# Kernel optimization log

Measured on AMD Instinct MI355X. Metric: run time of the kernel, lower is better.

## Reference

```python
import jax, jax.numpy as jnp
import numpy as np

BLOCK_SIZE = 128  # config.block_size; first query block skips intra-block causal mask (faithful to source)
NEG = -1e9       # the module uses -1e9, not -inf, for masking and m_i init


def setup_inputs() -> dict:
    key = jax.random.key(0)
    kq, kk, kv, km = jax.random.split(key, 4)
    B, S, H, D = 2, 2048, 16, 64
    q = jax.random.normal(kq, (B, S, H, D), dtype=jnp.float32)
    k = jax.random.normal(kk, (B, S, H, D), dtype=jnp.float32)
    v = jax.random.normal(kv, (B, S, H, D), dtype=jnp.float32)
    mask = jax.random.randint(km, (B, S), 0, 2).astype(bool)
    mask = mask.at[:, 0].set(True)  # keep first key attendable
    return {"q": q, "k": k, "v": v, "mask": mask}


def reference(q, k, v, mask):
    # q,k,v: [B,S,H,D]; mask: [B,S] bool (True = attend)
    B, S, H, D = q.shape
    scale = 1.0 / np.sqrt(D)
    # config.normalize_query=True -> F.normalize(q, dim=-1) (eps=1e-12)
    qn = q / jnp.maximum(jnp.linalg.norm(q, axis=-1, keepdims=True), 1e-12)
    # scores: [B,S(query),H,S(key)]
    scores = jnp.einsum('bshd,bkhd->bshk', qn, k) * scale
    qi = jnp.arange(S)[:, None]
    ki = jnp.arange(S)[None, :]
    # Faithful causal structure of the blocked PyTorch fallback:
    #  - keys limited to k <= q (triu(diagonal=block_start+1) masking)
    #  - EXCEPT the first query block (block_start==0), where the intra-block
    #    causal mask is skipped (keys still limited to the first block).
    allowed = (ki <= qi) | ((qi < BLOCK_SIZE) & (ki < BLOCK_SIZE))  # [S,S]
    scores = jnp.where(allowed[None, :, None, :], scores, NEG)
    scores = jnp.where(mask[:, None, None, :], scores, NEG)
    p = jax.nn.softmax(scores, axis=-1)
    out = jnp.einsum('bshk,bkhd->bshd', p, v)
    return out
```

## Files before the change

kernel.cpp:

```cpp
#include <hip/hip_runtime.h>
#include <stdint.h>

typedef __attribute__((ext_vector_type(8))) short short8;
typedef __attribute__((ext_vector_type(4))) float floatx4;
typedef __attribute__((ext_vector_type(4))) unsigned int uintx4;
typedef __attribute__((ext_vector_type(2))) unsigned int uintx2;

#define S_LEN 2048
#define NHEAD 16
#define DHEAD 64
#define KB    64
#define NTILE 32
#define PL_BYTES (S_LEN * DHEAD * 2)
#define VOFF  (2 * NHEAD * PL_BYTES)
#define MOFF  (2 * VOFF)
#define POFF  (MOFF + 8192)
#define DOFF  (POFF + 1024 * 16384)
#define WS_NEEDED ((size_t)DOFF + 1024 * 256)
#define NEGINF (-__builtin_inff())
#define LOG2E 1.4426950408889634f

#define GLOAD_LDS16(gp, lp) \
    __builtin_amdgcn_global_load_lds((const __attribute__((address_space(1))) unsigned int*)(gp), \
                                     (__attribute__((address_space(3))) unsigned int*)(lp), 16, 0, 0)

static __device__ __forceinline__ unsigned f2bf(float f) {
    union { float f; unsigned u; } w; w.f = f;
    return (w.u + 0x7FFFu + ((w.u >> 16) & 1u)) >> 16;
}

static __device__ __forceinline__ unsigned cvtpk(float lo, float hi) {
    unsigned r;
    asm("v_cvt_pk_bf16_f32 %0, %1, %2" : "=v"(r) : "v"(lo), "v"(hi));
    return r;
}

static __device__ __forceinline__ floatx4 mfma16(short8 a, short8 b, floatx4 c) {
    return __builtin_amdgcn_mfma_f32_16x16x32_bf16(a, b, c, 0, 0, 0);
}

__global__ __launch_bounds__(256) void prep_kernel(
    const float* __restrict__ kg, const float* __restrict__ vg,
    const int* __restrict__ mg, char* __restrict__ ws)
{
    __shared__ unsigned short Tl[64 * 72];
    const int bid = blockIdx.x;
    const int t   = bid & 31;
    const int bh  = bid >> 5;
    const int b   = bh >> 4, h = bh & 15;
    const int tid = threadIdx.x;
    char* kpre = ws + (size_t)bh * PL_BYTES;
    char* vpre = ws + VOFF + (size_t)bh * PL_BYTES;

    {
        const int r  = tid >> 2;
        const int c0 = (tid & 3) * 32;
        const int X  = (r & 7) << 4;
        const size_t grow = (((size_t)b * S_LEN + t * 64 + r) * NHEAD + h) * DHEAD;
        #pragma unroll
        for (int cc = 0; cc < 2; ++cc) {
            const int c  = c0 + 16 * cc;
            const int d0 = (c ^ X) >> 1;
            floatx4 f0 = *(const floatx4*)(kg + grow + d0);
            floatx4 f1 = *(const floatx4*)(kg + grow + d0 + 4);
            uintx4 pk = (uintx4){ f2bf(f0[0]) | (f2bf(f0[1]) << 16),
                                  f2bf(f0[2]) | (f2bf(f0[3]) << 16),
                                  f2bf(f1[0]) | (f2bf(f1[1]) << 16),
                                  f2bf(f1[2]) | (f2bf(f1[3]) << 16) };
            *(uintx4*)(kpre + t * 8192 + r * 128 + c) = pk;
        }
    }
    {
        const int key = tid >> 2;
        const int d0  = (tid & 3) * 16;
        const float vz = mg[(size_t)b * S_LEN + t * 64 + key] ? 1.f : 0.f;
        const size_t grow = (((size_t)b * S_LEN + t * 64 + key) * NHEAD + h) * DHEAD;
        #pragma unroll
        for (int q = 0; q < 4; ++q) {
            floatx4 f = *(const floatx4*)(vg + grow + d0 + 4 * q);
            #pragma unroll
            for (int ii = 0; ii < 4; ++ii)
                Tl[(d0 + 4 * q + ii) * 72 + key] = (unsigned short)f2bf(f[ii] * vz);
        }
    }
    __syncthreads();
    {
        const int d  = tid >> 2;
        const int c0 = (tid & 3) * 32;
        const int Xv = (d & 7) << 4;
        #pragma unroll
        for (int cc = 0; cc < 2; ++cc) {
            const int c   = c0 + 16 * cc;
            const int pp0 = (c ^ Xv) >> 1;
            const int blk = pp0 >> 5;
            const int a   = (pp0 & 31) >> 3;
            unsigned short vals[8];
            #pragma unroll
            for (int i = 0; i < 8; ++i) {
                const int key = 32 * blk + ((i < 4) ? (4 * a + i) : (16 + 4 * a + i - 4));
                vals[i] = Tl[d * 72 + key];
            }
            *(uintx4*)(vpre + t * 8192 + d * 128 + c) = *(const uintx4*)vals;
        }
    }
    if (h == 0 && tid < 64) {
        const int key = tid;
        const int gg = (key >> 2) & 3, lo = key & 3;
        const int ks = key >> 5,      hi = (key >> 4) & 1;
        const unsigned short mv = mg[(size_t)b * S_LEN + t * 64 + key] ? 0x3F80 : 0;
        *(unsigned short*)(ws + MOFF + (size_t)b * 4096 + t * 128
                           + gg * 32 + ks * 16 + (4 * hi + lo) * 2) = mv;
    }
}

__global__ __launch_bounds__(256, 4) void fa3_main(
    const float* __restrict__ qg, char* __restrict__ ws,
    float* __restrict__ og)
{
    __shared__ char smem[40960];
    unsigned short* Qs = (unsigned short*)smem;
    char* KsB = smem + 8192;
    char* VsB = smem + 24576;

    const int tid  = threadIdx.x;
    const int bid  = blockIdx.x;
    int a, bh, chunk;
    if (bid < 1024) { a = 31 - (bid >> 6); chunk = (bid >> 5) & 1; bh = bid & 31; }
    else            { int r = bid - 1024; a = 15 - (r >> 5); chunk = 0; bh = r & 31; }
    const int b    = bh >> 4;
    const int h    = bh & 15;
    const int w    = tid >> 6;
    const int lane = tid & 63;
    const int g    = lane >> 4;
    const int lm   = lane & 15;
    const int kh   = w >> 1;
    const int wq   = w & 1;
    const char* kpre = ws + (size_t)bh * PL_BYTES;
    const char* vpre = ws + VOFF + (size_t)bh * PL_BYTES;
    const char* mgf  = ws + MOFF + (size_t)b * 4096;

    const int nktTot = (a < 2) ? 2 : (a + 1);
    const bool split = (a >= 16);
    int kt0, kt1;
    if (split) {
        const int h1 = nktTot >> 1, h0 = nktTot - h1;
        kt0 = chunk ? h0 : 0;  kt1 = chunk ? nktTot : h0;
    } else { kt0 = 0; kt1 = nktTot; }

    {
        const size_t tb = (size_t)kt0 * 8192;
        GLOAD_LDS16(kpre + tb + tid * 16,        KsB + tid * 16);
        GLOAD_LDS16(kpre + tb + 4096 + tid * 16, KsB + 4096 + tid * 16);
        GLOAD_LDS16(vpre + tb + tid * 16,        VsB + tid * 16);
        GLOAD_LDS16(vpre + tb + 4096 + tid * 16, VsB + 4096 + tid * 16);
    }

    {
        const int r  = tid >> 2;
        const int q0 = tid & 3;
        const float* src = qg + (((size_t)b * S_LEN + (size_t)a * 64 + r) * NHEAD + h) * DHEAD + q0 * 16;
        floatx4 f0 = *(const floatx4*)(src + 0);
        floatx4 f1 = *(const floatx4*)(src + 4);
        floatx4 f2 = *(const floatx4*)(src + 8);
        floatx4 f3 = *(const floatx4*)(src + 12);
        float ssq = 0.f;
        #pragma unroll
        for (int i = 0; i < 4; ++i)
            ssq += f0[i]*f0[i] + f1[i]*f1[i] + f2[i]*f2[i] + f3[i]*f3[i];
        ssq += __shfl_xor(ssq, 1);
        ssq += __shfl_xor(ssq, 2);
        const float sc = (0.125f * LOG2E) / fmaxf(sqrtf(ssq), 1e-12f);
        float fv[16];
        #pragma unroll
        for (int i = 0; i < 4; ++i) { fv[i]=f0[i]; fv[4+i]=f1[i]; fv[8+i]=f2[i]; fv[12+i]=f3[i]; }
        unsigned pk[8];
        #pragma unroll
        for (int i = 0; i < 8; ++i)
            pk[i] = cvtpk(fv[2*i]*sc, fv[2*i+1]*sc);
        const int X = (r & 7) << 4;
        char* qp = (char*)Qs + r * 128;
        *(uintx4*)(qp + ((32*q0)      ^ X)) = (uintx4){pk[0],pk[1],pk[2],pk[3]};
        *(uintx4*)(qp + ((32*q0 + 16) ^ X)) = (uintx4){pk[4],pk[5],pk[6],pk[7]};
    }
    asm volatile("s_waitcnt vmcnt(0)" ::: "memory");
    __syncthreads();

    const int Xl = (lm & 7) << 4;
    short8 qf[2][2];
    #pragma unroll
    for (int grp = 0; grp < 2; ++grp) {
        const int row = wq * 32 + grp * 16 + lm;
        const char* base = (const char*)Qs + row * 128;
        #pragma unroll
        for (int ksd = 0; ksd < 2; ++ksd)
            qf[grp][ksd] = *(const short8*)(base + ((64*ksd + 16*g) ^ Xl));
    }

    floatx4 oacc[2][4];
    floatx4 dacc[2];
    #pragma unroll
    for (int grp = 0; grp < 2; ++grp) {
        dacc[grp] = (floatx4){0.f,0.f,0.f,0.f};
        #pragma unroll
        for (int nt = 0; nt < 4; ++nt) oacc[grp][nt] = (floatx4){0.f,0.f,0.f,0.f};
    }
    floatx4 NEG8 = (floatx4){-8.f,-8.f,-8.f,-8.f};
    asm volatile("" : "+v"(NEG8));
    const int qgl0 = a * 64 + wq * 32 + lm;

    int cur = 0;
    for (int kt = kt0; kt < kt1; ++kt) {
        if (kt + 1 < kt1) {
            const size_t tb = (size_t)(kt + 1) * 8192;
            char* kb = KsB + (cur ^ 1) * 8192;
            char* vb = VsB + (cur ^ 1) * 8192;
            GLOAD_LDS16(kpre + tb + tid * 16,        kb + tid * 16);
            GLOAD_LDS16(kpre + tb + 4096 + tid * 16, kb + 4096 + tid * 16);
            GLOAD_LDS16(vpre + tb + tid * 16,        vb + tid * 16);
            GLOAD_LDS16(vpre + tb + 4096 + tid * 16, vb + 4096 + tid * 16);
        }
        const short8 mf = *(const short8*)(mgf + kt * 128 + g * 32 + kh * 16);

        floatx4 st[2][2];
        const char* kbase = KsB + cur * 8192 + kh * 4096 + lm * 128;
        __builtin_amdgcn_s_setprio(1);
        #pragma unroll
        for (int mt = 0; mt < 2; ++mt) {
            short8 kf = *(const short8*)(kbase + mt * 2048 + ((16*g) ^ Xl));
            st[0][mt] = mfma16(kf, qf[0][0], NEG8);
            st[1][mt] = mfma16(kf, qf[1][0], NEG8);
        }
        #pragma unroll
        for (int mt = 0; mt < 2; ++mt) {
            short8 kf = *(const short8*)(kbase + mt * 2048 + ((64 + 16*g) ^ Xl));
            st[0][mt] = mfma16(kf, qf[0][1], st[0][mt]);
            st[1][mt] = mfma16(kf, qf[1][1], st[1][mt]);
        }
        __builtin_amdgcn_s_setprio(0);

        if ((a >= 2) && (kt == a)) {
            #pragma unroll
            for (int mt = 0; mt < 2; ++mt)
                #pragma unroll
                for (int j = 0; j < 4; ++j) {
                    const int kgl = kt * KB + kh * 32 + mt * 16 + 4 * g + j;
                    if (kgl > qgl0)      st[0][mt][j] = -10000.f;
                    if (kgl > qgl0 + 16) st[1][mt][j] = -10000.f;
                }
        }

        short8 pa[2];
        #pragma unroll
        for (int grp = 0; grp < 2; ++grp) {
            float p[8];
            #pragma unroll
            for (int mt = 0; mt < 2; ++mt)
                #pragma unroll
                for (int j = 0; j < 4; ++j)
                    p[mt * 4 + j] = exp2f(st[grp][mt][j]);
            union { short8 s; uintx4 u; } pu;
            pu.u = (uintx4){ cvtpk(p[0], p[1]), cvtpk(p[2], p[3]),
                             cvtpk(p[4], p[5]), cvtpk(p[6], p[7]) };
            pa[grp] = pu.s;
        }
        __builtin_amdgcn_s_setprio(1);
        dacc[0] = mfma16(pa[0], mf, dacc[0]);
        dacc[1] = mfma16(pa[1], mf, dacc[1]);
        {
            const char* vbase = VsB + cur * 8192 + lm * 128;
            #pragma unroll
            for (int nt = 0; nt < 4; ++nt) {
                short8 vf = *(const short8*)(vbase + nt * 2048 + ((64*kh + 16*g) ^ Xl));
                oacc[0][nt] = mfma16(pa[0], vf, oacc[0][nt]);
                oacc[1][nt] = mfma16(pa[1], vf, oacc[1][nt]);
            }
        }
        __builtin_amdgcn_s_setprio(0);

        asm volatile("s_waitcnt vmcnt(0)" ::: "memory");
        __syncthreads();
        cur ^= 1;
    }

    floatx4* rbuf = (floatx4*)(smem + 8192);
    float*   dbuf = (float*)smem;
    if (kh == 1) {
        #pragma unroll
        for (int grp = 0; grp < 2; ++grp)
            #pragma unroll
            for (int nt = 0; nt < 4; ++nt)
                rbuf[((grp * 4 + nt) * 2 + wq) * 64 + lane] = oacc[grp][nt];
    }
    __syncthreads();
    if (kh == 0) {
        #pragma unroll
        for (int grp = 0; grp < 2; ++grp)
            #pragma unroll
            for (int nt = 0; nt < 4; ++nt)
                oacc[grp][nt] += rbuf[((grp * 4 + nt) * 2 + wq) * 64 + lane];
    }
    __syncthreads();
    if (kh == 1 && lm == 0) {
        #pragma unroll
        for (int grp = 0; grp < 2; ++grp)
            #pragma unroll
            for (int j = 0; j < 4; ++j)
                dbuf[wq * 32 + grp * 16 + 4 * g + j] = dacc[grp][j];
    }
    __syncthreads();
    if (kh == 0) {
        if (!split) {
            #pragma unroll
            for (int grp = 0; grp < 2; ++grp)
                #pragma unroll
                for (int j = 0; j < 4; ++j) {
                    const int rl = wq * 32 + grp * 16 + 4 * g + j;
                    const float invj = 1.0f / (dacc[grp][j] + dbuf[rl]);
                    float* dst = og + (((size_t)b * S_LEN + a * 64 + rl) * NHEAD + h) * DHEAD + lm;
                    #pragma unroll
                    for (int nt = 0; nt < 4; ++nt) dst[nt * 16] = oacc[grp][nt][j] * invj;
                }
        } else {
            const int s = (((a & 15) * 32 + bh) << 1) | chunk;
            float* po = (float*)(ws + POFF + (size_t)s * 16384);
            float* pd = (float*)(ws + DOFF + (size_t)s * 256);
            #pragma unroll
            for (int grp = 0; grp < 2; ++grp)
                #pragma unroll
                for (int j = 0; j < 4; ++j) {
                    const int rl = wq * 32 + grp * 16 + 4 * g + j;
                    #pragma unroll
                    for (int nt = 0; nt < 4; ++nt)
                        po[rl * 64 + nt * 16 + lm] = oacc[grp][nt][j];
                    if (lm == 0) pd[rl] = dacc[grp][j] + dbuf[rl];
                }
        }
    }
}

__global__ __launch_bounds__(256) void fa3_combine(
    const char* __restrict__ ws, float* __restrict__ og)
{
    const int i0  = (blockIdx.x * 256 + threadIdx.x) * 8;
    const int d   = i0 & 63;
    const int row = (i0 >> 6) & 63;
    const int bh  = (i0 >> 12) & 31;
    const int ai  = i0 >> 17;
    const int b   = bh >> 4, h = bh & 15;
    const int s0  = ((ai * 32 + bh) << 1);
    const float* p0 = (const float*)(ws + POFF + (size_t)s0 * 16384) + row * 64 + d;
    const float* p1 = (const float*)(ws + POFF + (size_t)(s0 + 1) * 16384) + row * 64 + d;
    const float den = ((const float*)(ws + DOFF + (size_t)s0 * 256))[row]
                    + ((const float*)(ws + DOFF + (size_t)(s0 + 1) * 256))[row];
    const float inv = 1.0f / den;
    floatx4 a0 = *(const floatx4*)p0, a1 = *(const floatx4*)(p0 + 4);
    floatx4 b0 = *(const floatx4*)p1, b1 = *(const floatx4*)(p1 + 4);
    floatx4 o0, o1;
    #pragma unroll
    for (int i = 0; i < 4; ++i) { o0[i] = (a0[i] + b0[i]) * inv; o1[i] = (a1[i] + b1[i]) * inv; }
    float* dst = og + (((size_t)b * S_LEN + (16 + ai) * 64 + row) * NHEAD + h) * DHEAD + d;
    *(floatx4*)dst       = o0;
    *(floatx4*)(dst + 4) = o1;
}

__global__ __launch_bounds__(512) void fa3_fallback(
    const float* __restrict__ qg, const float* __restrict__ kg,
    const float* __restrict__ vg, const int* __restrict__ mg,
    float* __restrict__ og)
{
    __shared__ unsigned short Qs[128 * DHEAD];
    __shared__ unsigned short Ks2[KB * DHEAD];
    __shared__ unsigned short Vt[DHEAD * KB];
    __shared__ float Ms[KB];

    const int tid  = threadIdx.x;
    const int bid  = blockIdx.x;
    const int qb   = 15 - (bid >> 5);
    const int bh   = bid & 31;
    const int b    = bh >> 4;
    const int h    = bh & 15;
    const int w    = tid >> 6;
    const int lane = tid & 63;
    const int g    = lane >> 4;
    const int lm   = lane & 15;

    {
        const int r  = tid >> 2;
        const int q0 = tid & 3;
        const float* src = qg + (((size_t)b * S_LEN + (size_t)qb * 128 + r) * NHEAD + h) * DHEAD + q0 * 16;
        floatx4 f0 = *(const floatx4*)(src + 0);
        floatx4 f1 = *(const floatx4*)(src + 4);
        floatx4 f2 = *(const floatx4*)(src + 8);
        floatx4 f3 = *(const floatx4*)(src + 12);
        float ssq = 0.f;
        #pragma unroll
        for (int i = 0; i < 4; ++i)
            ssq += f0[i]*f0[i] + f1[i]*f1[i] + f2[i]*f2[i] + f3[i]*f3[i];
        ssq += __shfl_xor(ssq, 1);
        ssq += __shfl_xor(ssq, 2);
        const float sc = 0.125f / fmaxf(sqrtf(ssq), 1e-12f);
        float fv[16];
        #pragma unroll
        for (int i = 0; i < 4; ++i) { fv[i]=f0[i]; fv[4+i]=f1[i]; fv[8+i]=f2[i]; fv[12+i]=f3[i]; }
        unsigned pk[8];
        #pragma unroll
        for (int i = 0; i < 8; ++i)
            pk[i] = f2bf(fv[2*i]*sc) | (f2bf(fv[2*i+1]*sc) << 16);
        const int X = (r & 7) << 4;
        char* qp = (char*)Qs + r * 128;
        *(uintx4*)(qp + ((32*q0)      ^ X)) = (uintx4){pk[0],pk[1],pk[2],pk[3]};
        *(uintx4*)(qp + ((32*q0 + 16) ^ X)) = (uintx4){pk[4],pk[5],pk[6],pk[7]};
    }
    __syncthreads();

    short8 qf[2];
    {
        const int row = w * 16 + lm;
        const int X = (row & 7) << 4;
        const char* base = (const char*)Qs + row * 128;
        #pragma unroll
        for (int ks = 0; ks < 2; ++ks) {
            union { short8 s; uintx2 u[2]; } u;
            u.u[0] = *(const uintx2*)(base + ((64*ks + 8*g)      ^ X));
            u.u[1] = *(const uintx2*)(base + ((64*ks + 8*g + 32) ^ X));
            qf[ks] = u.s;
        }
    }

    floatx4 oacc[4];
    #pragma unroll
    for (int nt = 0; nt < 4; ++nt) oacc[nt] = (floatx4){0.f,0.f,0.f,0.f};
    float mrun = NEGINF, lrun = 0.f;
    const int q_glob = qb * 128 + w * 16 + lm;
    const int nkt = (qb == 0) ? 2 : (2 * qb + 2);

    for (int kt = 0; kt < nkt; ++kt) {
        const int kb0 = kt * KB;
        {
            const int r = tid >> 3;
            const int o = tid & 7;
            const size_t goff = (((size_t)b * S_LEN + kb0 + r) * NHEAD + h) * DHEAD + o * 8;
            floatx4 a0 = *(const floatx4*)(kg + goff);
            floatx4 a1 = *(const floatx4*)(kg + goff + 4);
            floatx4 c0 = *(const floatx4*)(vg + goff);
            floatx4 c1 = *(const floatx4*)(vg + goff + 4);
            uintx4 kw = (uintx4){ f2bf(a0[0]) | (f2bf(a0[1])<<16),
                                  f2bf(a0[2]) | (f2bf(a0[3])<<16),
                                  f2bf(a1[0]) | (f2bf(a1[1])<<16),
                                  f2bf(a1[2]) | (f2bf(a1[3])<<16) };
            *(uintx4*)((char*)Ks2 + r*128 + ((16*o) ^ ((r & 7) << 4))) = kw;
            float cv[8];
            #pragma unroll
            for (int i = 0; i < 4; ++i) { cv[i] = c0[i]; cv[4+i] = c1[i]; }
            #pragma unroll
            for (int i = 0; i < 8; ++i) {
                const int d = 8*o + i;
                Vt[d*64 + (r ^ (((i ^ o) & 7) << 3))] = (unsigned short)f2bf(cv[i]);
            }
            if (tid < KB) Ms[tid] = mg[(size_t)b * S_LEN + kb0 + tid] ? 0.f : NEGINF;
        }
        __syncthreads();

        floatx4 st[4];
        #pragma unroll
        for (int mt = 0; mt < 4; ++mt) st[mt] = (floatx4){0.f,0.f,0.f,0.f};
        #pragma unroll
        for (int ks = 0; ks < 2; ++ks) {
            #pragma unroll
            for (int mt = 0; mt < 4; ++mt) {
                const int row = mt * 16 + lm;
                const int X = (row & 7) << 4;
                const char* base = (const char*)Ks2 + row * 128;
                union { short8 s; uintx2 u[2]; } u;
                u.u[0] = *(const uintx2*)(base + ((64*ks + 8*g)      ^ X));
                u.u[1] = *(const uintx2*)(base + ((64*ks + 8*g + 32) ^ X));
                st[mt] = mfma16(u.s, qf[ks], st[mt]);
            }
        }

        const bool diag = (qb > 0) && (kt >= 2 * qb);
        float sv[16];
        #pragma unroll
        for (int mt = 0; mt < 4; ++mt) {
            #pragma unroll
            for (int j = 0; j < 4; ++j) {
                const int kl = mt * 16 + 4 * g + j;
                float s = st[mt][j] + Ms[kl];
                if (diag && (kb0 + kl > q_glob)) s = NEGINF;
                sv[mt * 4 + j] = s;
            }
        }

        float rmax = sv[0];
        #pragma unroll
        for (int i = 1; i < 16; ++i) rmax = fmaxf(rmax, sv[i]);
        rmax = fmaxf(rmax, __shfl_xor(rmax, 16));
        rmax = fmaxf(rmax, __shfl_xor(rmax, 32));
        const float mnew = fmaxf(mrun, rmax);
        const float cf = __expf(mrun - mnew);
        float p[16], psum = 0.f;
        #pragma unroll
        for (int i = 0; i < 16; ++i) { p[i] = __expf(sv[i] - mnew); psum += p[i]; }
        psum += __shfl_xor(psum, 16);
        psum += __shfl_xor(psum, 32);
        lrun = lrun * cf + psum;
        mrun = mnew;

        float cj[4];
        #pragma unroll
        for (int j = 0; j < 4; ++j) cj[j] = __shfl(cf, 20 * g + j);
        #pragma unroll
        for (int nt = 0; nt < 4; ++nt)
            #pragma unroll
            for (int j = 0; j < 4; ++j) oacc[nt][j] *= cj[j];

        short8 pa[2];
        #pragma unroll
        for (int ks = 0; ks < 2; ++ks)
            #pragma unroll
            for (int i = 0; i < 8; ++i)
                pa[ks][i] = (short)f2bf(p[(2*ks + (i>>2))*4 + (i&3)]);

        #pragma unroll
        for (int nt = 0; nt < 4; ++nt) {
            const int d = 16 * nt + lm;
            const int xz = (((d & 7) ^ ((d >> 3) & 7)) & 7) << 4;
            const char* vb = (const char*)Vt + d * 128;
            #pragma unroll
            for (int ks = 0; ks < 2; ++ks) {
                union { short8 s; uintx2 u[2]; } vu;
                vu.u[0] = *(const uintx2*)(vb + ((64*ks + 8*g)      ^ xz));
                vu.u[1] = *(const uintx2*)(vb + ((64*ks + 8*g + 32) ^ xz));
                oacc[nt] = mfma16(pa[ks], vu.s, oacc[nt]);
            }
        }
        __syncthreads();
    }

    const float inv = 1.0f / lrun;
    #pragma unroll
    for (int j = 0; j < 4; ++j) {
        const float invj = __shfl(inv, 20 * g + j);
        const int row = qb * 128 + w * 16 + 4 * g + j;
        float* dst = og + (((size_t)b * S_LEN + row) * NHEAD + h) * DHEAD + lm;
        #pragma unroll
        for (int nt = 0; nt < 4; ++nt) dst[nt * 16] = oacc[nt][j] * invj;
    }
}

extern "C" void kernel_launch(void* const* d_in, const int* in_sizes, int n_in,
                              void* d_out, int out_size, void* d_ws, size_t ws_size,
                              hipStream_t stream)
{
    const float* q = (const float*)d_in[0];
    const float* k = (const float*)d_in[1];
    const float* v = (const float*)d_in[2];
    const int*   m = (const int*)d_in[3];
    float* out = (float*)d_out;
    (void)in_sizes; (void)n_in; (void)out_size;
    if (ws_size >= WS_NEEDED) {
        prep_kernel<<<dim3(1024), dim3(256), 0, stream>>>(k, v, m, (char*)d_ws);
        fa3_main<<<dim3(1536), dim3(256), 0, stream>>>(q, (char*)d_ws, out);
        fa3_combine<<<dim3(1024), dim3(256), 0, stream>>>((const char*)d_ws, out);
    } else {
        fa3_fallback<<<dim3(512), dim3(512), 0, stream>>>(q, k, v, m, out);
    }
}
```

Measured before the change: 52.66 us.

## Use FP8 QK^T MFMA with 128-row query blocks and 512-thread workgroups

```diff
diff --git a/kernel.cpp b/kernel.cpp
--- a/kernel.cpp
+++ b/kernel.cpp
@@ -10,15 +10,16 @@
 #define NHEAD 16
 #define DHEAD 64
 #define KB    64
-#define NTILE 32
-#define PL_BYTES (S_LEN * DHEAD * 2)
-#define VOFF  (2 * NHEAD * PL_BYTES)
-#define MOFF  (2 * VOFF)
+#define KPL   131072
+#define VPL   262144
+#define VOFF  (32 * KPL)
+#define MOFF  (VOFF + 32 * VPL)
 #define POFF  (MOFF + 8192)
-#define DOFF  (POFF + 1024 * 16384)
-#define WS_NEEDED ((size_t)DOFF + 1024 * 256)
+#define DOFF  (POFF + 512 * 32768)
+#define WS_NEEDED ((size_t)DOFF + 512 * 512)
 #define NEGINF (-__builtin_inff())
 #define LOG2E 1.4426950408889634f
+#define CSC   0.011271055f
 
 #define GLOAD_LDS16(gp, lp) \
     __builtin_amdgcn_global_load_lds((const __attribute__((address_space(1))) unsigned int*)(gp), \
@@ -28,15 +29,20 @@
     union { float f; unsigned u; } w; w.f = f;
     return (w.u + 0x7FFFu + ((w.u >> 16) & 1u)) >> 16;
 }
-
 static __device__ __forceinline__ unsigned cvtpk(float lo, float hi) {
     unsigned r;
     asm("v_cvt_pk_bf16_f32 %0, %1, %2" : "=v"(r) : "v"(lo), "v"(hi));
     return r;
 }
-
+template <int HI>
+static __device__ __forceinline__ int cvtfp8(float a, float b, int old) {
+    return __builtin_amdgcn_cvt_pk_fp8_f32(a, b, old, HI);
+}
 static __device__ __forceinline__ floatx4 mfma16(short8 a, short8 b, floatx4 c) {
     return __builtin_amdgcn_mfma_f32_16x16x32_bf16(a, b, c, 0, 0, 0);
+}
+static __device__ __forceinline__ floatx4 mfma8(long a, long b, floatx4 c) {
+    return __builtin_amdgcn_mfma_f32_16x16x32_fp8_fp8(a, b, c, 0, 0, 0);
 }
 
 __global__ __launch_bounds__(256) void prep_kernel(
@@ -49,26 +55,27 @@
     const int bh  = bid >> 5;
     const int b   = bh >> 4, h = bh & 15;
     const int tid = threadIdx.x;
-    char* kpre = ws + (size_t)bh * PL_BYTES;
-    char* vpre = ws + VOFF + (size_t)bh * PL_BYTES;
+    char* kpre = ws + (size_t)bh * KPL;
+    char* vpre = ws + VOFF + (size_t)bh * VPL;
 
     {
         const int r  = tid >> 2;
-        const int c0 = (tid & 3) * 32;
-        const int X  = (r & 7) << 4;
-        const size_t grow = (((size_t)b * S_LEN + t * 64 + r) * NHEAD + h) * DHEAD;
-        #pragma unroll
-        for (int cc = 0; cc < 2; ++cc) {
-            const int c  = c0 + 16 * cc;
-            const int d0 = (c ^ X) >> 1;
-            floatx4 f0 = *(const floatx4*)(kg + grow + d0);
-            floatx4 f1 = *(const floatx4*)(kg + grow + d0 + 4);
-            uintx4 pk = (uintx4){ f2bf(f0[0]) | (f2bf(f0[1]) << 16),
-                                  f2bf(f0[2]) | (f2bf(f0[3]) << 16),
-                                  f2bf(f1[0]) | (f2bf(f1[1]) << 16),
-                                  f2bf(f1[2]) | (f2bf(f1[3]) << 16) };
-            *(uintx4*)(kpre + t * 8192 + r * 128 + c) = pk;
-        }
+        const int c4 = tid & 3;
+        const size_t grow = (((size_t)b * S_LEN + t * 64 + r) * NHEAD + h) * DHEAD + 16 * c4;
+        floatx4 f0 = *(const floatx4*)(kg + grow);
+        floatx4 f1 = *(const floatx4*)(kg + grow + 4);
+        floatx4 f2 = *(const floatx4*)(kg + grow + 8);
+        floatx4 f3 = *(const floatx4*)(kg + grow + 12);
+        int w0 = 0, w1 = 0, w2 = 0, w3 = 0;
+        w0 = cvtfp8<0>(f0[0], f0[1], w0); w0 = cvtfp8<1>(f0[2], f0[3], w0);
+        w1 = cvtfp8<0>(f1[0], f1[1], w1); w1 = cvtfp8<1>(f1[2], f1[3], w1);
+        w2 = cvtfp8<0>(f2[0], f2[1], w2); w2 = cvtfp8<1>(f2[2], f2[3], w2);
+        w3 = cvtfp8<0>(f3[0], f3[1], w3); w3 = cvtfp8<1>(f3[2], f3[3], w3);
+        const int Xr = r & 7;
+        char* dst = kpre + t * 4096 + r * 64 + 8 * (((2 * c4) ^ Xr) & ~1);
+        *(uintx4*)dst = (Xr & 1)
+            ? (uintx4){(unsigned)w2, (unsigned)w3, (unsigned)w0, (unsigned)w1}
+            : (uintx4){(unsigned)w0, (unsigned)w1, (unsigned)w2, (unsigned)w3};
     }
     {
         const int key = tid >> 2;
@@ -113,52 +120,44 @@
     }
 }
 
-__global__ __launch_bounds__(256, 4) void fa3_main(
+__global__ __launch_bounds__(512, 4) void fa3_main(
     const float* __restrict__ qg, char* __restrict__ ws,
     float* __restrict__ og)
 {
-    __shared__ char smem[40960];
-    unsigned short* Qs = (unsigned short*)smem;
+    __shared__ char smem[32768];
+    char* Qs  = smem;
     char* KsB = smem + 8192;
-    char* VsB = smem + 24576;
+    char* VsB = smem + 16384;
 
     const int tid  = threadIdx.x;
     const int bid  = blockIdx.x;
-    int a, bh, chunk;
-    if (bid < 1024) { a = 31 - (bid >> 6); chunk = (bid >> 5) & 1; bh = bid & 31; }
-    else            { int r = bid - 1024; a = 15 - (r >> 5); chunk = 0; bh = r & 31; }
+    const int gidx = bid >> 5;
+    const int bh   = bid & 31;
+    int qb, chunk; bool split;
+    if (gidx < 16) { qb = 15 - (gidx >> 1); chunk = gidx & 1; split = true; }
+    else           { qb = 7 - (gidx - 16);  chunk = 0;        split = false; }
     const int b    = bh >> 4;
     const int h    = bh & 15;
     const int w    = tid >> 6;
     const int lane = tid & 63;
     const int g    = lane >> 4;
     const int lm   = lane & 15;
-    const int kh   = w >> 1;
-    const int wq   = w & 1;
-    const char* kpre = ws + (size_t)bh * PL_BYTES;
-    const char* vpre = ws + VOFF + (size_t)bh * PL_BYTES;
+    const int kh   = w >> 2;
+    const int wq   = w & 3;
+    const char* kpre = ws + (size_t)bh * KPL;
+    const char* vpre = ws + VOFF + (size_t)bh * VPL;
     const char* mgf  = ws + MOFF + (size_t)b * 4096;
-
-    const int nktTot = (a < 2) ? 2 : (a + 1);
-    const bool split = (a >= 16);
-    int kt0, kt1;
-    if (split) {
-        const int h1 = nktTot >> 1, h0 = nktTot - h1;
-        kt0 = chunk ? h0 : 0;  kt1 = chunk ? nktTot : h0;
-    } else { kt0 = 0; kt1 = nktTot; }
-
-    {
-        const size_t tb = (size_t)kt0 * 8192;
-        GLOAD_LDS16(kpre + tb + tid * 16,        KsB + tid * 16);
-        GLOAD_LDS16(kpre + tb + 4096 + tid * 16, KsB + 4096 + tid * 16);
-        GLOAD_LDS16(vpre + tb + tid * 16,        VsB + tid * 16);
-        GLOAD_LDS16(vpre + tb + 4096 + tid * 16, VsB + 4096 + tid * 16);
-    }
+    const int nkt = (qb == 0) ? 2 : (2 * qb + 2);
+    int kt0 = 0, kt1 = nkt;
+    if (split) { const int hh = nkt >> 1; kt0 = chunk ? hh : 0; kt1 = chunk ? nkt : hh; }
+
+    if (tid < 256) GLOAD_LDS16(kpre + (size_t)kt0 * 4096 + tid * 16, KsB + tid * 16);
+    GLOAD_LDS16(vpre + (size_t)kt0 * 8192 + tid * 16, VsB + tid * 16);
 
     {
         const int r  = tid >> 2;
         const int q0 = tid & 3;
-        const float* src = qg + (((size_t)b * S_LEN + (size_t)a * 64 + r) * NHEAD + h) * DHEAD + q0 * 16;
+        const float* src = qg + (((size_t)b * S_LEN + (size_t)qb * 128 + r) * NHEAD + h) * DHEAD + q0 * 16;
         floatx4 f0 = *(const floatx4*)(src + 0);
         floatx4 f1 = *(const floatx4*)(src + 4);
         floatx4 f2 = *(const floatx4*)(src + 8);
@@ -169,31 +168,30 @@
             ssq += f0[i]*f0[i] + f1[i]*f1[i] + f2[i]*f2[i] + f3[i]*f3[i];
         ssq += __shfl_xor(ssq, 1);
         ssq += __shfl_xor(ssq, 2);
-        const float sc = (0.125f * LOG2E) / fmaxf(sqrtf(ssq), 1e-12f);
-        float fv[16];
-        #pragma unroll
-        for (int i = 0; i < 4; ++i) { fv[i]=f0[i]; fv[4+i]=f1[i]; fv[8+i]=f2[i]; fv[12+i]=f3[i]; }
-        unsigned pk[8];
-        #pragma unroll
-        for (int i = 0; i < 8; ++i)
-            pk[i] = cvtpk(fv[2*i]*sc, fv[2*i+1]*sc);
-        const int X = (r & 7) << 4;
-        char* qp = (char*)Qs + r * 128;
-        *(uintx4*)(qp + ((32*q0)      ^ X)) = (uintx4){pk[0],pk[1],pk[2],pk[3]};
-        *(uintx4*)(qp + ((32*q0 + 16) ^ X)) = (uintx4){pk[4],pk[5],pk[6],pk[7]};
+        const float sc = 16.0f / fmaxf(sqrtf(ssq), 1e-12f);
+        int w0 = 0, w1 = 0, w2 = 0, w3 = 0;
+        w0 = cvtfp8<0>(f0[0]*sc, f0[1]*sc, w0); w0 = cvtfp8<1>(f0[2]*sc, f0[3]*sc, w0);
+        w1 = cvtfp8<0>(f1[0]*sc, f1[1]*sc, w1); w1 = cvtfp8<1>(f1[2]*sc, f1[3]*sc, w1);
+        w2 = cvtfp8<0>(f2[0]*sc, f2[1]*sc, w2); w2 = cvtfp8<1>(f2[2]*sc, f2[3]*sc, w2);
+        w3 = cvtfp8<0>(f3[0]*sc, f3[1]*sc, w3); w3 = cvtfp8<1>(f3[2]*sc, f3[3]*sc, w3);
+        const int Xr = r & 7;
+        char* qp = Qs + r * 64 + 8 * (((2 * q0) ^ Xr) & ~1);
+        *(uintx4*)qp = (Xr & 1)
+            ? (uintx4){(unsigned)w2, (unsigned)w3, (unsigned)w0, (unsigned)w1}
+            : (uintx4){(unsigned)w0, (unsigned)w1, (unsigned)w2, (unsigned)w3};
     }
     asm volatile("s_waitcnt vmcnt(0)" ::: "memory");
     __syncthreads();
 
-    const int Xl = (lm & 7) << 4;
-    short8 qf[2][2];
+    const int Xl8  = (lm & 7) << 3;
+    const int Xl16 = (lm & 7) << 4;
+    long qf8[2][2];
     #pragma unroll
     for (int grp = 0; grp < 2; ++grp) {
-        const int row = wq * 32 + grp * 16 + lm;
-        const char* base = (const char*)Qs + row * 128;
+        const char* base = Qs + (wq * 32 + grp * 16 + lm) * 64;
         #pragma unroll
         for (int ksd = 0; ksd < 2; ++ksd)
-            qf[grp][ksd] = *(const short8*)(base + ((64*ksd + 16*g) ^ Xl));
+            qf8[grp][ksd] = *(const long*)(base + ((32 * ksd + 8 * g) ^ Xl8));
     }
 
     floatx4 oacc[2][4];
@@ -204,48 +202,46 @@
         #pragma unroll
         for (int nt = 0; nt < 4; ++nt) oacc[grp][nt] = (floatx4){0.f,0.f,0.f,0.f};
     }
-    floatx4 NEG8 = (floatx4){-8.f,-8.f,-8.f,-8.f};
-    asm volatile("" : "+v"(NEG8));
-    const int qgl0 = a * 64 + wq * 32 + lm;
+    floatx4 ZERO4 = (floatx4){0.f,0.f,0.f,0.f};
+    asm volatile("" : "+v"(ZERO4));
+    const int qgl0 = qb * 128 + wq * 32 + lm;
 
     int cur = 0;
     for (int kt = kt0; kt < kt1; ++kt) {
         if (kt + 1 < kt1) {
-            const size_t tb = (size_t)(kt + 1) * 8192;
-            char* kb = KsB + (cur ^ 1) * 8192;
-            char* vb = VsB + (cur ^ 1) * 8192;
-            GLOAD_LDS16(kpre + tb + tid * 16,        kb + tid * 16);
-            GLOAD_LDS16(kpre + tb + 4096 + tid * 16, kb + 4096 + tid * 16);
-            GLOAD_LDS16(vpre + tb + tid * 16,        vb + tid * 16);
-            GLOAD_LDS16(vpre + tb + 4096 + tid * 16, vb + 4096 + tid * 16);
+            if (tid < 256)
+                GLOAD_LDS16(kpre + (size_t)(kt + 1) * 4096 + tid * 16,
+                            KsB + (cur ^ 1) * 4096 + tid * 16);
+            GLOAD_LDS16(vpre + (size_t)(kt + 1) * 8192 + tid * 16,
+                        VsB + (cur ^ 1) * 8192 + tid * 16);
         }
         const short8 mf = *(const short8*)(mgf + kt * 128 + g * 32 + kh * 16);
 
         floatx4 st[2][2];
-        const char* kbase = KsB + cur * 8192 + kh * 4096 + lm * 128;
+        const char* kbase = KsB + cur * 4096 + kh * 2048 + lm * 64;
         __builtin_amdgcn_s_setprio(1);
         #pragma unroll
         for (int mt = 0; mt < 2; ++mt) {
-            short8 kf = *(const short8*)(kbase + mt * 2048 + ((16*g) ^ Xl));
-            st[0][mt] = mfma16(kf, qf[0][0], NEG8);
-            st[1][mt] = mfma16(kf, qf[1][0], NEG8);
+            long kf = *(const long*)(kbase + mt * 1024 + ((8 * g) ^ Xl8));
+            st[0][mt] = mfma8(kf, qf8[0][0], ZERO4);
+            st[1][mt] = mfma8(kf, qf8[1][0], ZERO4);
         }
         #pragma unroll
         for (int mt = 0; mt < 2; ++mt) {
-            short8 kf = *(const short8*)(kbase + mt * 2048 + ((64 + 16*g) ^ Xl));
-            st[0][mt] = mfma16(kf, qf[0][1], st[0][mt]);
-            st[1][mt] = mfma16(kf, qf[1][1], st[1][mt]);
+            long kf = *(const long*)(kbase + mt * 1024 + ((32 + 8 * g) ^ Xl8));
+            st[0][mt] = mfma8(kf, qf8[0][1], st[0][mt]);
+            st[1][mt] = mfma8(kf, qf8[1][1], st[1][mt]);
         }
         __builtin_amdgcn_s_setprio(0);
 
-        if ((a >= 2) && (kt == a)) {
+        if ((qb >= 1) && (kt >= 2 * qb)) {
             #pragma unroll
             for (int mt = 0; mt < 2; ++mt)
                 #pragma unroll
                 for (int j = 0; j < 4; ++j) {
                     const int kgl = kt * KB + kh * 32 + mt * 16 + 4 * g + j;
-                    if (kgl > qgl0)      st[0][mt][j] = -10000.f;
-                    if (kgl > qgl0 + 16) st[1][mt][j] = -10000.f;
+                    if (kgl > qgl0)      st[0][mt][j] = -1e6f;
+                    if (kgl > qgl0 + 16) st[1][mt][j] = -1e6f;
                 }
         }
 
@@ -257,7 +253,7 @@
             for (int mt = 0; mt < 2; ++mt)
                 #pragma unroll
                 for (int j = 0; j < 4; ++j)
-                    p[mt * 4 + j] = exp2f(st[grp][mt][j]);
+                    p[mt * 4 + j] = exp2f(fmaf(st[grp][mt][j], CSC, -8.0f));
             union { short8 s; uintx4 u; } pu;
             pu.u = (uintx4){ cvtpk(p[0], p[1]), cvtpk(p[2], p[3]),
                              cvtpk(p[4], p[5]), cvtpk(p[6], p[7]) };
@@ -270,7 +266,7 @@
             const char* vbase = VsB + cur * 8192 + lm * 128;
             #pragma unroll
             for (int nt = 0; nt < 4; ++nt) {
-                short8 vf = *(const short8*)(vbase + nt * 2048 + ((64*kh + 16*g) ^ Xl));
+                short8 vf = *(const short8*)(vbase + nt * 2048 + ((64 * kh + 16 * g) ^ Xl16));
                 oacc[0][nt] = mfma16(pa[0], vf, oacc[0][nt]);
                 oacc[1][nt] = mfma16(pa[1], vf, oacc[1][nt]);
             }
@@ -282,14 +278,14 @@
         cur ^= 1;
     }
 
-    floatx4* rbuf = (floatx4*)(smem + 8192);
+    floatx4* rbuf = (floatx4*)smem;
     float*   dbuf = (float*)smem;
     if (kh == 1) {
         #pragma unroll
         for (int grp = 0; grp < 2; ++grp)
             #pragma unroll
             for (int nt = 0; nt < 4; ++nt)
-                rbuf[((grp * 4 + nt) * 2 + wq) * 64 + lane] = oacc[grp][nt];
+                rbuf[((grp * 4 + nt) * 4 + wq) * 64 + lane] = oacc[grp][nt];
     }
     __syncthreads();
     if (kh == 0) {
@@ -297,7 +293,7 @@
         for (int grp = 0; grp < 2; ++grp)
             #pragma unroll
             for (int nt = 0; nt < 4; ++nt)
-                oacc[grp][nt] += rbuf[((grp * 4 + nt) * 2 + wq) * 64 + lane];
+                oacc[grp][nt] += rbuf[((grp * 4 + nt) * 4 + wq) * 64 + lane];
     }
     __syncthreads();
     if (kh == 1 && lm == 0) {
@@ -316,14 +312,14 @@
                 for (int j = 0; j < 4; ++j) {
                     const int rl = wq * 32 + grp * 16 + 4 * g + j;
                     const float invj = 1.0f / (dacc[grp][j] + dbuf[rl]);
-                    float* dst = og + (((size_t)b * S_LEN + a * 64 + rl) * NHEAD + h) * DHEAD + lm;
+                    float* dst = og + (((size_t)b * S_LEN + qb * 128 + rl) * NHEAD + h) * DHEAD + lm;
                     #pragma unroll
                     for (int nt = 0; nt < 4; ++nt) dst[nt * 16] = oacc[grp][nt][j] * invj;
                 }
         } else {
-            const int s = (((a & 15) * 32 + bh) << 1) | chunk;
-            float* po = (float*)(ws + POFF + (size_t)s * 16384);
-            float* pd = (float*)(ws + DOFF + (size_t)s * 256);
+            const int s = ((qb - 8) * 32 + bh) * 2 + chunk;
+            float* po = (float*)(ws + POFF + (size_t)s * 32768);
+            float* pd = (float*)(ws + DOFF + (size_t)s * 512);
             #pragma unroll
             for (int grp = 0; grp < 2; ++grp)
                 #pragma unroll
@@ -343,22 +339,22 @@
 {
     const int i0  = (blockIdx.x * 256 + threadIdx.x) * 8;
     const int d   = i0 & 63;
-    const int row = (i0 >> 6) & 63;
-    const int bh  = (i0 >> 12) & 31;
-    const int ai  = i0 >> 17;
+    const int row = (i0 >> 6) & 127;
+    const int bh  = (i0 >> 13) & 31;
+    const int qbi = i0 >> 18;
     const int b   = bh >> 4, h = bh & 15;
-    const int s0  = ((ai * 32 + bh) << 1);
-    const float* p0 = (const float*)(ws + POFF + (size_t)s0 * 16384) + row * 64 + d;
-    const float* p1 = (const float*)(ws + POFF + (size_t)(s0 + 1) * 16384) + row * 64 + d;
-    const float den = ((const float*)(ws + DOFF + (size_t)s0 * 256))[row]
-                    + ((const float*)(ws + DOFF + (size_t)(s0 + 1) * 256))[row];
+    const int s0  = (qbi * 32 + bh) * 2;
+    const float* p0 = (const float*)(ws + POFF + (size_t)s0 * 32768) + row * 64 + d;
+    const float* p1 = (const float*)(ws + POFF + (size_t)(s0 + 1) * 32768) + row * 64 + d;
+    const float den = ((const float*)(ws + DOFF + (size_t)s0 * 512))[row]
+                    + ((const float*)(ws + DOFF + (size_t)(s0 + 1) * 512))[row];
     const float inv = 1.0f / den;
     floatx4 a0 = *(const floatx4*)p0, a1 = *(const floatx4*)(p0 + 4);
     floatx4 b0 = *(const floatx4*)p1, b1 = *(const floatx4*)(p1 + 4);
     floatx4 o0, o1;
     #pragma unroll
     for (int i = 0; i < 4; ++i) { o0[i] = (a0[i] + b0[i]) * inv; o1[i] = (a1[i] + b1[i]) * inv; }
-    float* dst = og + (((size_t)b * S_LEN + (16 + ai) * 64 + row) * NHEAD + h) * DHEAD + d;
+    float* dst = og + (((size_t)b * S_LEN + (8 + qbi) * 128 + row) * NHEAD + h) * DHEAD + d;
     *(floatx4*)dst       = o0;
     *(floatx4*)(dst + 4) = o1;
 }
@@ -560,7 +556,7 @@
     (void)in_sizes; (void)n_in; (void)out_size;
     if (ws_size >= WS_NEEDED) {
         prep_kernel<<<dim3(1024), dim3(256), 0, stream>>>(k, v, m, (char*)d_ws);
-        fa3_main<<<dim3(1536), dim3(256), 0, stream>>>(q, (char*)d_ws, out);
+        fa3_main<<<dim3(768), dim3(512), 0, stream>>>(q, (char*)d_ws, out);
         fa3_combine<<<dim3(1024), dim3(256), 0, stream>>>((const char*)d_ws, out);
     } else {
         fa3_fallback<<<dim3(512), dim3(512), 0, stream>>>(q, k, v, m, out);
```

Result: slower. 56.17 us (+6.7%).
